# Kernel optimization log

Measured on AMD Instinct MI355X. Metric: run time of the kernel, lower is better.

The kernel has to match this reference:

```python
import jax, jax.numpy as jnp
import numpy as np

E = 2048      # embedding_size
H = 16        # num_heads
D = 128       # head_dim
G = 4         # gqa_factor
KH = H // G   # kv heads
F = 8192      # up_proj_size
B, S = 2, 2048


def _layer_norm(x, g, b, eps=1e-5):
    mu = jnp.mean(x, axis=-1, keepdims=True)
    var = jnp.mean(jnp.square(x - mu), axis=-1, keepdims=True)
    return (x - mu) * jax.lax.rsqrt(var + eps) * g + b


def setup_inputs() -> dict:
    key = jax.random.key(0)
    ks = jax.random.split(key, 16)
    std = 0.02
    inp = {
        'x': jax.random.normal(ks[0], (B, S, E), dtype=jnp.float32),
        'ln1_g': jnp.ones((E,), jnp.float32),
        'ln1_b': jnp.zeros((E,), jnp.float32),
        'wq': jax.random.normal(ks[1], (E, H * D), jnp.float32) * std,
        'bq': jnp.zeros((H * D,), jnp.float32),
        'wk': jax.random.normal(ks[2], (E, KH * D), jnp.float32) * std,
        'bk': jnp.zeros((KH * D,), jnp.float32),
        'wv': jax.random.normal(ks[3], (E, KH * D), jnp.float32) * std,
        'bv': jnp.zeros((KH * D,), jnp.float32),
        'wo': jax.random.normal(ks[4], (H * D, E), jnp.float32) * std,
        'bo': jnp.zeros((E,), jnp.float32),
        'ln2_g': jnp.ones((E,), jnp.float32),
        'ln2_b': jnp.zeros((E,), jnp.float32),
        'wu': jax.random.normal(ks[5], (E, F), jnp.float32) * std,
        'bu': jnp.zeros((F,), jnp.float32),
        'wd': jax.random.normal(ks[6], (F, E), jnp.float32) * std,
        'bd': jnp.zeros((E,), jnp.float32),
    }
    return inp


def _block(x, ln1_g, ln1_b, wq, bq, wk, bk, wv, bv, wo, bo, ln2_g, ln2_b, wu, bu, wd, bd):
    b, s, e = x.shape
    # attention sub-block (use_cache=False, train_mode=False -> no dropout)
    x1 = _layer_norm(x, ln1_g, ln1_b)
    q = (x1 @ wq + bq).reshape(b, s, H, D).transpose(0, 2, 1, 3)       # (B,H,S,D)
    q = q.reshape(b, KH, G, s, D)                                       # (B,KH,G,S,D)
    k = (x1 @ wk + bk).reshape(b, s, KH, D).transpose(0, 2, 1, 3)      # (B,KH,S,D)
    v = (x1 @ wv + bv).reshape(b, s, KH, D).transpose(0, 2, 1, 3)      # (B,KH,S,D)
    scores = jnp.einsum('bkgsd,bktd->bkgst', q, k) / np.sqrt(D).astype(np.float32)
    causal = jnp.tril(jnp.ones((s, s), dtype=bool))                     # True = keep
    scores = jnp.where(causal, scores, -jnp.inf)
    att = jax.nn.softmax(scores, axis=-1)
    o = jnp.einsum('bkgst,bktd->bkgsd', att, v)                         # (B,KH,G,S,D)
    o = o.reshape(b, H, s, D).transpose(0, 2, 1, 3).reshape(b, s, H * D)
    x = x + (o @ wo + bo)
    # MLP sub-block
    x2 = _layer_norm(x, ln2_g, ln2_b)
    h = jax.nn.gelu(x2 @ wu + bu, approximate=False)
    x = x + (h @ wd + bd)
    return x


def reference(x, ln1_g, ln1_b, wq, bq, wk, bk, wv, bv, wo, bo, ln2_g, ln2_b, wu, bu, wd, bd):
    return _block(x, ln1_g, ln1_b, wq, bq, wk, bk, wv, bv, wo, bo, ln2_g, ln2_b, wu, bu, wd, bd)
```

## Files before the change

kernel.cpp:

```cpp
#include <hip/hip_runtime.h>
#include <hip/hip_bf16.h>
#include <cstdint>
#include <math.h>

typedef unsigned short u16;
using f32x4   = __attribute__((ext_vector_type(4))) float;
using short8  = __attribute__((ext_vector_type(8))) short;
using short4v = __attribute__((ext_vector_type(4))) short;

#define DEV static __device__ __forceinline__

DEV u16 f2bf(float f) {
  union { float f; unsigned u; } v; v.f = f;
  unsigned r = v.u + 0x7fffu + ((v.u >> 16) & 1u);
  return (u16)(r >> 16);
}

DEV f32x4 mfma_bf16(short8 a, short8 b, f32x4 c) {
  return __builtin_amdgcn_mfma_f32_16x16x32_bf16(a, b, c, 0, 0, 0);
}

DEV void gload16(const void* g, void* l) {
  __builtin_amdgcn_global_load_lds((const __attribute__((address_space(1))) void*)g,
                                   (__attribute__((address_space(3))) void*)l,
                                   16, 0, 0);
}

__global__ __launch_bounds__(256) void transpose_cvt(
    const float* __restrict__ in, u16* __restrict__ out, int K, int N)
{
  __shared__ float tile[32][33];
  const int n0 = blockIdx.x * 32, k0 = blockIdx.y * 32;
  const int c = threadIdx.x & 31, r = threadIdx.x >> 5;
#pragma unroll
  for (int i = 0; i < 4; i++) {
    const int row = r + i * 8;
    tile[row][c] = in[(size_t)(k0 + row) * N + n0 + c];
  }
  __syncthreads();
#pragma unroll
  for (int i = 0; i < 4; i++) {
    const int row = r + i * 8;
    out[(size_t)(n0 + row) * K + k0 + c] = f2bf(tile[c][row]);
  }
}

__global__ __launch_bounds__(256) void ln_kernel(
    const float* __restrict__ x, const float* __restrict__ g,
    const float* __restrict__ bt, u16* __restrict__ out)
{
  __shared__ float red1[4], red2[4];
  const int row = blockIdx.x;
  const int t = threadIdx.x;
  const int lane = t & 63, w = t >> 6;
  const float* xr = x + (size_t)row * 2048 + t * 8;
  float v[8];
  {
    const float4* p4 = (const float4*)xr;
    float4 a = p4[0], b = p4[1];
    v[0] = a.x; v[1] = a.y; v[2] = a.z; v[3] = a.w;
    v[4] = b.x; v[5] = b.y; v[6] = b.z; v[7] = b.w;
  }
  float s = 0.f;
#pragma unroll
  for (int j = 0; j < 8; j++) s += v[j];
#pragma unroll
  for (int m = 1; m < 64; m <<= 1) s += __shfl_xor(s, m);
  if (lane == 0) red1[w] = s;
  __syncthreads();
  const float mu = (red1[0] + red1[1] + red1[2] + red1[3]) * (1.f / 2048.f);
  float q = 0.f;
#pragma unroll
  for (int j = 0; j < 8; j++) { v[j] -= mu; q += v[j] * v[j]; }
#pragma unroll
  for (int m = 1; m < 64; m <<= 1) q += __shfl_xor(q, m);
  if (lane == 0) red2[w] = q;
  __syncthreads();
  const float rstd = rsqrtf((red2[0] + red2[1] + red2[2] + red2[3]) * (1.f / 2048.f) + 1e-5f);
  const float4* g4 = (const float4*)(g + t * 8);
  const float4* b4 = (const float4*)(bt + t * 8);
  float4 ga = g4[0], gb = g4[1], ba = b4[0], bb = b4[1];
  float gg[8] = {ga.x, ga.y, ga.z, ga.w, gb.x, gb.y, gb.z, gb.w};
  float bbv[8] = {ba.x, ba.y, ba.z, ba.w, bb.x, bb.y, bb.z, bb.w};
  short8 o;
#pragma unroll
  for (int j = 0; j < 8; j++) o[j] = (short)f2bf(v[j] * rstd * gg[j] + bbv[j]);
  *(short8*)&out[(size_t)row * 2048 + t * 8] = o;
}

template<int MODE, int N, int K>
__global__ void __launch_bounds__(256) gemm_bt(
    const u16* __restrict__ A, const u16* __restrict__ Bt,
    const float* __restrict__ bias, const float* __restrict__ resid,
    u16* __restrict__ out_bf, float* __restrict__ out_f)
{
  __shared__ u16 As[128 * 64];
  __shared__ u16 Bs[128 * 64];
  const int m0 = blockIdx.y * 128;
  const int n0 = blockIdx.x * 128;
  const int tid = threadIdx.x;
  const int lane = tid & 63, w = tid >> 6;
  const int wm = w >> 1, wn = w & 1;
  const int z = lane >> 4, l15 = lane & 15;

  f32x4 acc[4][4];
#pragma unroll
  for (int m = 0; m < 4; m++)
#pragma unroll
    for (int n = 0; n < 4; n++)
#pragma unroll
      for (int i = 0; i < 4; i++) acc[m][n][i] = 0.f;

  for (int k0 = 0; k0 < K; k0 += 64) {
#pragma unroll
    for (int j = 0; j < 4; j++) {
      const int seg = w * 4 + j;
      const int c = seg * 64 + lane;
      const int r = c >> 3;
      const int cc = (c & 7) ^ (r & 7);
      gload16(A + (size_t)(m0 + r) * K + k0 + cc * 8, &As[seg * 512]);
    }
#pragma unroll
    for (int j = 0; j < 4; j++) {
      const int seg = w * 4 + j;
      const int c = seg * 64 + lane;
      const int r = c >> 3;
      const int cc = (c & 7) ^ (r & 7);
      gload16(Bt + (size_t)(n0 + r) * K + k0 + cc * 8, &Bs[seg * 512]);
    }
    asm volatile("s_waitcnt vmcnt(0)" ::: "memory");
    __syncthreads();

#pragma unroll
    for (int kk = 0; kk < 2; kk++) {
      short8 af[4], bfr[4];
#pragma unroll
      for (int m = 0; m < 4; m++) {
        const int row = wm * 64 + m * 16 + l15;
        const int off = row * 64 + ((kk * 32 + z * 8) ^ ((row & 7) << 3));
        af[m] = *(const short8*)&As[off];
      }
#pragma unroll
      for (int n = 0; n < 4; n++) {
        const int row = wn * 64 + n * 16 + l15;
        const int off = row * 64 + ((kk * 32 + z * 8) ^ ((row & 7) << 3));
        bfr[n] = *(const short8*)&Bs[off];
      }
#pragma unroll
      for (int m = 0; m < 4; m++)
#pragma unroll
        for (int n = 0; n < 4; n++)
          acc[m][n] = mfma_bf16(af[m], bfr[n], acc[m][n]);
    }
    __syncthreads();
  }

#pragma unroll
  for (int m = 0; m < 4; m++) {
    const int row0 = m0 + wm * 64 + m * 16 + z * 4;
#pragma unroll
    for (int n = 0; n < 4; n++) {
      const int col = n0 + wn * 64 + n * 16 + l15;
      f32x4 v = acc[m][n];
      const float bb = bias[col];
      if constexpr (MODE == 0) {
#pragma unroll
        for (int i = 0; i < 4; i++)
          out_bf[(size_t)(row0 + i) * N + col] = f2bf((v[i] + bb) * 0.08838834764831845f);
      } else if constexpr (MODE == 1) {
#pragma unroll
        for (int i = 0; i < 4; i++)
          out_bf[(size_t)(row0 + i) * N + col] = f2bf(v[i] + bb);
      } else if constexpr (MODE == 2) {
        const int bidx = row0 >> 11, sidx = row0 & 2047;
        const int kh = col >> 7, d = col & 127;
        short4v p;
#pragma unroll
        for (int i = 0; i < 4; i++) p[i] = (short)f2bf(v[i] + bb);
        *(short4v*)&out_bf[(size_t)((bidx * 4 + kh) * 128 + d) * 2048 + sidx] = p;
      } else if constexpr (MODE == 3) {
#pragma unroll
        for (int i = 0; i < 4; i++) {
          const size_t idx = (size_t)(row0 + i) * N + col;
          out_f[idx] = v[i] + bb + resid[idx];
        }
      } else if constexpr (MODE == 4) {
#pragma unroll
        for (int i = 0; i < 4; i++) {
          const float xx = v[i] + bb;
          out_bf[(size_t)(row0 + i) * N + col] =
              f2bf(0.5f * xx * (1.f + erff(xx * 0.70710678118654752f)));
        }
      } else {
#pragma unroll
        for (int i = 0; i < 4; i++) {
          const size_t idx = (size_t)(row0 + i) * N + col;
          out_f[idx] = v[i] + bb + out_f[idx];
        }
      }
    }
  }
}

__global__ void __launch_bounds__(256) attn_kernel(
    const u16* __restrict__ qb, const u16* __restrict__ kb,
    const u16* __restrict__ vt, u16* __restrict__ ob)
{
  __shared__ u16 Kt[64 * 128];
  __shared__ u16 Vs[128 * 64];
  __shared__ u16 Pl[4 * 32 * 64];

  const int qt = blockIdx.x;
  const int bh = blockIdx.y;
  const int b = bh >> 4, h = bh & 15, kh = h >> 2;
  const int q0 = qt * 128;
  const int tid = threadIdx.x, lane = tid & 63, w = tid >> 6;
  const int z = lane >> 4, l15 = lane & 15;
  const int qw0 = q0 + w * 32;

  short8 qf[2][4];
#pragma unroll
  for (int m = 0; m < 2; m++)
#pragma unroll
    for (int kk = 0; kk < 4; kk++)
      qf[m][kk] = *(const short8*)&qb[(size_t)(b * 2048 + qw0 + m * 16 + l15) * 2048 +
                                      h * 128 + kk * 32 + z * 8];

  f32x4 oacc[2][8];
#pragma unroll
  for (int m = 0; m < 2; m++)
#pragma unroll
    for (int n = 0; n < 8; n++)
#pragma unroll
      for (int i = 0; i < 4; i++) oacc[m][n][i] = 0.f;
  float mst[2][4], lst[2][4];
#pragma unroll
  for (int m = 0; m < 2; m++)
#pragma unroll
    for (int i = 0; i < 4; i++) { mst[m][i] = -1e30f; lst[m][i] = 0.f; }

  const int ntiles = q0 / 64 + 2;
  for (int t = 0; t < ntiles; t++) {
    const int kv0 = t * 64;
#pragma unroll
    for (int j = 0; j < 4; j++) {
      const int seg = w * 4 + j;
      const int c = seg * 64 + lane;
      const int r = c >> 4;
      const int cc = (c & 15) ^ (r & 7);
      gload16(kb + (size_t)(b * 2048 + kv0 + r) * 512 + kh * 128 + cc * 8, &Kt[seg * 512]);
    }
#pragma unroll
    for (int j = 0; j < 4; j++) {
      const int seg = w * 4 + j;
      const int c = seg * 64 + lane;
      const int d = c >> 3;
      const int cc = (c & 7) ^ (d & 7);
      gload16(vt + (size_t)((b * 4 + kh) * 128 + d) * 2048 + kv0 + cc * 8, &Vs[seg * 512]);
    }
    asm volatile("s_waitcnt vmcnt(0)" ::: "memory");
    __syncthreads();

    f32x4 sf[2][4];
#pragma unroll
    for (int m = 0; m < 2; m++)
#pragma unroll
      for (int n = 0; n < 4; n++)
#pragma unroll
        for (int i = 0; i < 4; i++) sf[m][n][i] = 0.f;

#pragma unroll
    for (int kk = 0; kk < 4; kk++) {
      short8 kfr[4];
#pragma unroll
      for (int n = 0; n < 4; n++) {
        const int row = n * 16 + l15;
        const int off = row * 128 + ((kk * 32 + z * 8) ^ ((row & 7) << 3));
        kfr[n] = *(const short8*)&Kt[off];
      }
#pragma unroll
      for (int m = 0; m < 2; m++)
#pragma unroll
        for (int n = 0; n < 4; n++)
          sf[m][n] = mfma_bf16(qf[m][kk], kfr[n], sf[m][n]);
    }

    u16* Pw = &Pl[w * 2048];
#pragma unroll
    for (int m = 0; m < 2; m++) {
#pragma unroll
      for (int i = 0; i < 4; i++) {
        const int rq = qw0 + m * 16 + z * 4 + i;
#pragma unroll
        for (int n = 0; n < 4; n++)
          if (kv0 + n * 16 + l15 > rq) sf[m][n][i] = -1e30f;
        float mx = fmaxf(fmaxf(sf[m][0][i], sf[m][1][i]), fmaxf(sf[m][2][i], sf[m][3][i]));
        mx = fmaxf(mx, __shfl_xor(mx, 1));
        mx = fmaxf(mx, __shfl_xor(mx, 2));
        mx = fmaxf(mx, __shfl_xor(mx, 4));
        mx = fmaxf(mx, __shfl_xor(mx, 8));
        const float mn = fmaxf(mst[m][i], mx);
        const float al = __expf(mst[m][i] - mn);
        mst[m][i] = mn;
        float rs = 0.f;
#pragma unroll
        for (int n = 0; n < 4; n++) {
          const float p = __expf(sf[m][n][i] - mn);
          sf[m][n][i] = p;
          rs += p;
        }
        rs += __shfl_xor(rs, 1);
        rs += __shfl_xor(rs, 2);
        rs += __shfl_xor(rs, 4);
        rs += __shfl_xor(rs, 8);
        lst[m][i] = lst[m][i] * al + rs;
#pragma unroll
        for (int n = 0; n < 8; n++) oacc[m][n][i] *= al;
        const int prow = m * 16 + z * 4 + i;
#pragma unroll
        for (int n = 0; n < 4; n++)
          Pw[prow * 64 + ((n * 16 + l15) ^ ((prow & 7) << 3))] = f2bf(sf[m][n][i]);
      }
    }

#pragma unroll
    for (int kk = 0; kk < 2; kk++) {
      short8 af[2], vf[8];
#pragma unroll
      for (int m = 0; m < 2; m++) {
        const int row = m * 16 + l15;
        af[m] = *(const short8*)&Pw[row * 64 + ((kk * 32 + z * 8) ^ ((row & 7) << 3))];
      }
#pragma unroll
      for (int n = 0; n < 8; n++) {
        const int row = n * 16 + l15;
        vf[n] = *(const short8*)&Vs[row * 64 + ((kk * 32 + z * 8) ^ ((row & 7) << 3))];
      }
#pragma unroll
      for (int m = 0; m < 2; m++)
#pragma unroll
        for (int n = 0; n < 8; n++)
          oacc[m][n] = mfma_bf16(af[m], vf[n], oacc[m][n]);
    }
    __syncthreads();
  }

#pragma unroll
  for (int m = 0; m < 2; m++)
#pragma unroll
    for (int n = 0; n < 8; n++) {
      const int dcol = n * 16 + l15;
#pragma unroll
      for (int i = 0; i < 4; i++) {
        const int rq = qw0 + m * 16 + z * 4 + i;
        ob[(size_t)(b * 2048 + rq) * 2048 + h * 128 + dcol] = f2bf(oacc[m][n][i] / lst[m][i]);
      }
    }
}

extern "C" void kernel_launch(void* const* d_in, const int* in_sizes, int n_in,
                              void* d_out, int out_size, void* d_ws, size_t ws_size,
                              hipStream_t stream) {
  (void)in_sizes; (void)n_in; (void)out_size; (void)ws_size;
  const float* x     = (const float*)d_in[0];
  const float* ln1_g = (const float*)d_in[1];
  const float* ln1_b = (const float*)d_in[2];
  const float* wq    = (const float*)d_in[3];
  const float* bq    = (const float*)d_in[4];
  const float* wk    = (const float*)d_in[5];
  const float* bk    = (const float*)d_in[6];
  const float* wv    = (const float*)d_in[7];
  const float* bv    = (const float*)d_in[8];
  const float* wo    = (const float*)d_in[9];
  const float* bo    = (const float*)d_in[10];
  const float* ln2_g = (const float*)d_in[11];
  const float* ln2_b = (const float*)d_in[12];
  const float* wu    = (const float*)d_in[13];
  const float* bu    = (const float*)d_in[14];
  const float* wd    = (const float*)d_in[15];
  const float* bd    = (const float*)d_in[16];
  float* out = (float*)d_out;

  char* p = (char*)d_ws;
  u16* wqT = (u16*)p; p += (size_t)2048 * 2048 * 2;
  u16* wkT = (u16*)p; p += (size_t)512 * 2048 * 2;
  u16* wvT = (u16*)p; p += (size_t)512 * 2048 * 2;
  u16* woT = (u16*)p; p += (size_t)2048 * 2048 * 2;
  u16* wuT = (u16*)p; p += (size_t)8192 * 2048 * 2;
  u16* wdT = (u16*)p; p += (size_t)2048 * 8192 * 2;
  u16* x1  = (u16*)p; p += (size_t)4096 * 2048 * 2;
  u16* qbuf= (u16*)p; p += (size_t)4096 * 2048 * 2;
  u16* kbuf= (u16*)p; p += (size_t)4096 * 512 * 2;
  u16* vtb = (u16*)p; p += (size_t)4096 * 512 * 2;
  u16* hb  = (u16*)p; p += (size_t)4096 * 8192 * 2;
  u16* ob  = x1;
  u16* x2  = qbuf;

  transpose_cvt<<<dim3(64, 64),  256, 0, stream>>>(wq, wqT, 2048, 2048);
  transpose_cvt<<<dim3(16, 64),  256, 0, stream>>>(wk, wkT, 2048, 512);
  transpose_cvt<<<dim3(16, 64),  256, 0, stream>>>(wv, wvT, 2048, 512);
  transpose_cvt<<<dim3(64, 64),  256, 0, stream>>>(wo, woT, 2048, 2048);
  transpose_cvt<<<dim3(256, 64), 256, 0, stream>>>(wu, wuT, 2048, 8192);
  transpose_cvt<<<dim3(64, 256), 256, 0, stream>>>(wd, wdT, 8192, 2048);

  ln_kernel<<<4096, 256, 0, stream>>>(x, ln1_g, ln1_b, x1);

  gemm_bt<0, 2048, 2048><<<dim3(16, 32), 256, 0, stream>>>(x1, wqT, bq, nullptr, qbuf, nullptr);
  gemm_bt<1, 512,  2048><<<dim3(4, 32),  256, 0, stream>>>(x1, wkT, bk, nullptr, kbuf, nullptr);
  gemm_bt<2, 512,  2048><<<dim3(4, 32),  256, 0, stream>>>(x1, wvT, bv, nullptr, vtb,  nullptr);

  attn_kernel<<<dim3(16, 32), 256, 0, stream>>>(qbuf, kbuf, vtb, ob);

  gemm_bt<3, 2048, 2048><<<dim3(16, 32), 256, 0, stream>>>(ob, woT, bo, x, nullptr, out);

  ln_kernel<<<4096, 256, 0, stream>>>(out, ln2_g, ln2_b, x2);

  gemm_bt<4, 8192, 2048><<<dim3(64, 32), 256, 0, stream>>>(x2, wuT, bu, nullptr, hb, nullptr);
  gemm_bt<5, 2048, 8192><<<dim3(16, 32), 256, 0, stream>>>(hb, wdT, bd, nullptr, nullptr, out);
}
```

Before: 875.9 us.

## Double-buffer K/V tiles in attention, remap blocks by XCD, skip masked work

The attention kernel now double-buffers K and V tiles in LDS, so the global loads for the next tile overlap with compute on the current one. Blocks move to a 1D grid that groups each (batch, head) onto one XCD and pairs heavy and light causal query tiles for load balance. Waves skip tiles that are fully masked, apply the causal mask only on diagonal tiles, and rescale the accumulator only when the running max grows. It also adds s_setprio around the MFMA sections and uses one reciprocal per output row. The cost is double the LDS for K/V, which may lower occupancy.

```diff
diff --git a/kernel.cpp b/kernel.cpp
--- a/kernel.cpp
+++ b/kernel.cpp
@@ -206,17 +206,24 @@
     const u16* __restrict__ qb, const u16* __restrict__ kb,
     const u16* __restrict__ vt, u16* __restrict__ ob)
 {
-  __shared__ u16 Kt[64 * 128];
-  __shared__ u16 Vs[128 * 64];
+  __shared__ u16 Kt[2][64 * 128];
+  __shared__ u16 Vs[2][128 * 64];
   __shared__ u16 Pl[4 * 32 * 64];
 
-  const int qt = blockIdx.x;
-  const int bh = blockIdx.y;
+  const int idx = blockIdx.x;
+  const int xcd = idx & 7;
+  const int u = (idx >> 3) & 31;
+  const int half = idx >> 8;
+  const int bh = xcd * 4 + (u & 3);
+  const int qh = u >> 2;
+  const int qt = half ? (15 - qh) : qh;
+
   const int b = bh >> 4, h = bh & 15, kh = h >> 2;
   const int q0 = qt * 128;
   const int tid = threadIdx.x, lane = tid & 63, w = tid >> 6;
   const int z = lane >> 4, l15 = lane & 15;
   const int qw0 = q0 + w * 32;
+  const int ksw = (l15 & 7) << 3;
 
   short8 qf[2][4];
 #pragma unroll
@@ -239,16 +246,16 @@
 #pragma unroll
     for (int i = 0; i < 4; i++) { mst[m][i] = -1e30f; lst[m][i] = 0.f; }
 
-  const int ntiles = q0 / 64 + 2;
-  for (int t = 0; t < ntiles; t++) {
-    const int kv0 = t * 64;
+  auto STAGE = [&](int tt, int bufsel) {
+    const int kv0s = tt * 64;
 #pragma unroll
     for (int j = 0; j < 4; j++) {
       const int seg = w * 4 + j;
       const int c = seg * 64 + lane;
       const int r = c >> 4;
       const int cc = (c & 15) ^ (r & 7);
-      gload16(kb + (size_t)(b * 2048 + kv0 + r) * 512 + kh * 128 + cc * 8, &Kt[seg * 512]);
+      gload16(kb + (size_t)(b * 2048 + kv0s + r) * 512 + kh * 128 + cc * 8,
+              &Kt[bufsel][seg * 512]);
     }
 #pragma unroll
     for (int j = 0; j < 4; j++) {
@@ -256,105 +263,132 @@
       const int c = seg * 64 + lane;
       const int d = c >> 3;
       const int cc = (c & 7) ^ (d & 7);
-      gload16(vt + (size_t)((b * 4 + kh) * 128 + d) * 2048 + kv0 + cc * 8, &Vs[seg * 512]);
-    }
+      gload16(vt + (size_t)((b * 4 + kh) * 128 + d) * 2048 + kv0s + cc * 8,
+              &Vs[bufsel][seg * 512]);
+    }
+  };
+
+  const int ntiles = q0 / 64 + 2;
+
+  STAGE(0, 0);
+  asm volatile("s_waitcnt vmcnt(0)" ::: "memory");
+  __syncthreads();
+
+  for (int t = 0; t < ntiles; t++) {
+    const int cur = t & 1;
+    if (t + 1 < ntiles) STAGE(t + 1, cur ^ 1);
+
+    const int kv0 = t * 64;
+    if (kv0 <= qw0 + 31) {
+      f32x4 sf[2][4];
+#pragma unroll
+      for (int m = 0; m < 2; m++)
+#pragma unroll
+        for (int n = 0; n < 4; n++)
+#pragma unroll
+          for (int i = 0; i < 4; i++) sf[m][n][i] = 0.f;
+
+      __builtin_amdgcn_s_setprio(1);
+#pragma unroll
+      for (int kk = 0; kk < 4; kk++) {
+        short8 kfr[4];
+#pragma unroll
+        for (int n = 0; n < 4; n++) {
+          const int row = n * 16 + l15;
+          kfr[n] = *(const short8*)&Kt[cur][row * 128 + ((kk * 32 + z * 8) ^ ksw)];
+        }
+#pragma unroll
+        for (int m = 0; m < 2; m++)
+#pragma unroll
+          for (int n = 0; n < 4; n++)
+            sf[m][n] = mfma_bf16(qf[m][kk], kfr[n], sf[m][n]);
+      }
+      __builtin_amdgcn_s_setprio(0);
+
+      u16* Pw = &Pl[w * 2048];
+      const bool edge = (kv0 + 63 > qw0);
+#pragma unroll
+      for (int m = 0; m < 2; m++) {
+#pragma unroll
+        for (int i = 0; i < 4; i++) {
+          const int rq = qw0 + m * 16 + z * 4 + i;
+          if (edge) {
+#pragma unroll
+            for (int n = 0; n < 4; n++)
+              if (kv0 + n * 16 + l15 > rq) sf[m][n][i] = -1e30f;
+          }
+          float mx = fmaxf(fmaxf(sf[m][0][i], sf[m][1][i]), fmaxf(sf[m][2][i], sf[m][3][i]));
+          mx = fmaxf(mx, __shfl_xor(mx, 1));
+          mx = fmaxf(mx, __shfl_xor(mx, 2));
+          mx = fmaxf(mx, __shfl_xor(mx, 4));
+          mx = fmaxf(mx, __shfl_xor(mx, 8));
+          const bool grow = mx > mst[m][i];
+          const float mn = grow ? mx : mst[m][i];
+          float rs = 0.f;
+#pragma unroll
+          for (int n = 0; n < 4; n++) {
+            const float p = __expf(sf[m][n][i] - mn);
+            sf[m][n][i] = p;
+            rs += p;
+          }
+          rs += __shfl_xor(rs, 1);
+          rs += __shfl_xor(rs, 2);
+          rs += __shfl_xor(rs, 4);
+          rs += __shfl_xor(rs, 8);
+          if (grow) {
+            const float al = __expf(mst[m][i] - mx);
+            mst[m][i] = mx;
+            lst[m][i] = lst[m][i] * al + rs;
+#pragma unroll
+            for (int n = 0; n < 8; n++) oacc[m][n][i] *= al;
+          } else {
+            lst[m][i] += rs;
+          }
+          const int prow = m * 16 + z * 4 + i;
+          const int psw = ((z * 4 + i) & 7) << 3;
+#pragma unroll
+          for (int n = 0; n < 4; n++)
+            Pw[prow * 64 + ((n * 16 + l15) ^ psw)] = f2bf(sf[m][n][i]);
+        }
+      }
+
+      __builtin_amdgcn_s_setprio(1);
+#pragma unroll
+      for (int kk = 0; kk < 2; kk++) {
+        short8 af[2], vf[8];
+#pragma unroll
+        for (int m = 0; m < 2; m++) {
+          const int row = m * 16 + l15;
+          af[m] = *(const short8*)&Pw[row * 64 + ((kk * 32 + z * 8) ^ ksw)];
+        }
+#pragma unroll
+        for (int n = 0; n < 8; n++) {
+          const int row = n * 16 + l15;
+          vf[n] = *(const short8*)&Vs[cur][row * 64 + ((kk * 32 + z * 8) ^ ksw)];
+        }
+#pragma unroll
+        for (int m = 0; m < 2; m++)
+#pragma unroll
+          for (int n = 0; n < 8; n++)
+            oacc[m][n] = mfma_bf16(af[m], vf[n], oacc[m][n]);
+      }
+      __builtin_amdgcn_s_setprio(0);
+    }
+
     asm volatile("s_waitcnt vmcnt(0)" ::: "memory");
     __syncthreads();
-
-    f32x4 sf[2][4];
-#pragma unroll
-    for (int m = 0; m < 2; m++)
-#pragma unroll
-      for (int n = 0; n < 4; n++)
-#pragma unroll
-        for (int i = 0; i < 4; i++) sf[m][n][i] = 0.f;
-
-#pragma unroll
-    for (int kk = 0; kk < 4; kk++) {
-      short8 kfr[4];
-#pragma unroll
-      for (int n = 0; n < 4; n++) {
-        const int row = n * 16 + l15;
-        const int off = row * 128 + ((kk * 32 + z * 8) ^ ((row & 7) << 3));
-        kfr[n] = *(const short8*)&Kt[off];
-      }
-#pragma unroll
-      for (int m = 0; m < 2; m++)
-#pragma unroll
-        for (int n = 0; n < 4; n++)
-          sf[m][n] = mfma_bf16(qf[m][kk], kfr[n], sf[m][n]);
-    }
-
-    u16* Pw = &Pl[w * 2048];
-#pragma unroll
-    for (int m = 0; m < 2; m++) {
-#pragma unroll
-      for (int i = 0; i < 4; i++) {
-        const int rq = qw0 + m * 16 + z * 4 + i;
-#pragma unroll
-        for (int n = 0; n < 4; n++)
-          if (kv0 + n * 16 + l15 > rq) sf[m][n][i] = -1e30f;
-        float mx = fmaxf(fmaxf(sf[m][0][i], sf[m][1][i]), fmaxf(sf[m][2][i], sf[m][3][i]));
-        mx = fmaxf(mx, __shfl_xor(mx, 1));
-        mx = fmaxf(mx, __shfl_xor(mx, 2));
-        mx = fmaxf(mx, __shfl_xor(mx, 4));
-        mx = fmaxf(mx, __shfl_xor(mx, 8));
-        const float mn = fmaxf(mst[m][i], mx);
-        const float al = __expf(mst[m][i] - mn);
-        mst[m][i] = mn;
-        float rs = 0.f;
-#pragma unroll
-        for (int n = 0; n < 4; n++) {
-          const float p = __expf(sf[m][n][i] - mn);
-          sf[m][n][i] = p;
-          rs += p;
-        }
-        rs += __shfl_xor(rs, 1);
-        rs += __shfl_xor(rs, 2);
-        rs += __shfl_xor(rs, 4);
-        rs += __shfl_xor(rs, 8);
-        lst[m][i] = lst[m][i] * al + rs;
-#pragma unroll
-        for (int n = 0; n < 8; n++) oacc[m][n][i] *= al;
-        const int prow = m * 16 + z * 4 + i;
-#pragma unroll
-        for (int n = 0; n < 4; n++)
-          Pw[prow * 64 + ((n * 16 + l15) ^ ((prow & 7) << 3))] = f2bf(sf[m][n][i]);
-      }
-    }
-
-#pragma unroll
-    for (int kk = 0; kk < 2; kk++) {
-      short8 af[2], vf[8];
-#pragma unroll
-      for (int m = 0; m < 2; m++) {
-        const int row = m * 16 + l15;
-        af[m] = *(const short8*)&Pw[row * 64 + ((kk * 32 + z * 8) ^ ((row & 7) << 3))];
-      }
-#pragma unroll
-      for (int n = 0; n < 8; n++) {
-        const int row = n * 16 + l15;
-        vf[n] = *(const short8*)&Vs[row * 64 + ((kk * 32 + z * 8) ^ ((row & 7) << 3))];
-      }
-#pragma unroll
-      for (int m = 0; m < 2; m++)
-#pragma unroll
-        for (int n = 0; n < 8; n++)
-          oacc[m][n] = mfma_bf16(af[m], vf[n], oacc[m][n]);
-    }
-    __syncthreads();
   }
 
 #pragma unroll
   for (int m = 0; m < 2; m++)
 #pragma unroll
-    for (int n = 0; n < 8; n++) {
-      const int dcol = n * 16 + l15;
-#pragma unroll
-      for (int i = 0; i < 4; i++) {
-        const int rq = qw0 + m * 16 + z * 4 + i;
-        ob[(size_t)(b * 2048 + rq) * 2048 + h * 128 + dcol] = f2bf(oacc[m][n][i] / lst[m][i]);
-      }
+    for (int i = 0; i < 4; i++) {
+      const float inv = 1.0f / lst[m][i];
+      const int rq = qw0 + m * 16 + z * 4 + i;
+      u16* orow = &ob[(size_t)(b * 2048 + rq) * 2048 + h * 128];
+#pragma unroll
+      for (int n = 0; n < 8; n++)
+        orow[n * 16 + l15] = f2bf(oacc[m][n][i] * inv);
     }
 }
 
@@ -409,7 +443,7 @@
   gemm_bt<1, 512,  2048><<<dim3(4, 32),  256, 0, stream>>>(x1, wkT, bk, nullptr, kbuf, nullptr);
   gemm_bt<2, 512,  2048><<<dim3(4, 32),  256, 0, stream>>>(x1, wvT, bv, nullptr, vtb,  nullptr);
 
-  attn_kernel<<<dim3(16, 32), 256, 0, stream>>>(qbuf, kbuf, vtb, ob);
+  attn_kernel<<<512, 256, 0, stream>>>(qbuf, kbuf, vtb, ob);
 
   gemm_bt<3, 2048, 2048><<<dim3(16, 32), 256, 0, stream>>>(ob, woT, bo, x, nullptr, out);
 
```

Result: faster. 805.6 us (-8.0%).
